# Performance work log

Hardware: AMD Instinct MI355X
Metric: run time of the kernel (lower is better)

Reference implementation:

```python
import jax, jax.numpy as jnp
import numpy as np

B, T, D, H = 1, 4096, 1024, 16
HD = D // H          # head_dim = 64
W_LOCAL = 256        # sliding-window half-width (hardcoded in module)
N_GLOBAL = 64        # number of global tokens (hardcoded in module)


def setup_inputs() -> dict:
    key = jax.random.key(0)
    ks = jax.random.split(key, 7)
    s = 0.02
    return {
        "hidden_states": jax.random.normal(ks[0], (B, T, D), dtype=jnp.float32),
        "Wqkv": jax.random.normal(ks[1], (D, 3 * D), dtype=jnp.float32) * s,
        "bqkv": jnp.zeros((3 * D,), dtype=jnp.float32),
        "Wout": jax.random.normal(ks[2], (D, D), dtype=jnp.float32) * s,
        "bout": jnp.zeros((D,), dtype=jnp.float32),
        "Wg": jax.random.normal(ks[3], (D, 1), dtype=jnp.float32) * s,
        "bg": jnp.zeros((1,), dtype=jnp.float32),
    }


def reference(hidden_states, Wqkv, bqkv, Wout, bout, Wg, bg):
    b, t, d = hidden_states.shape
    scale = 1.0 / jnp.sqrt(jnp.asarray(HD, hidden_states.dtype))

    qkv = hidden_states @ Wqkv + bqkv                     # [B,T,3D]
    q, k, v = jnp.split(qkv, 3, axis=-1)
    # [B,T,D] -> [B,H,T,HD]
    q, k, v = (x.reshape(b, t, H, HD).transpose(0, 2, 1, 3) for x in (q, k, v))

    # local sliding-window attention (dense scores masked to |i-j| <= w, as in source)
    idx = jnp.arange(t)
    local_mask = jnp.abs(idx[None, :] - idx[:, None]) <= W_LOCAL   # [T,T]
    scores = jnp.einsum('bhqd,bhkd->bhqk', q, k) * scale           # [B,H,T,T]
    scores = jnp.where(local_mask[None, None], scores, -jnp.inf)
    attn_local = jnp.einsum('bhqk,bhkd->bhqd', jax.nn.softmax(scores, axis=-1), v)

    # global-token attention: every query attends to the first N_GLOBAL tokens
    ng = min(N_GLOBAL, t)
    k_g = k[:, :, :ng, :]                                          # [B,H,G,HD]
    v_g = v[:, :, :ng, :]
    scores_g = jnp.einsum('bhqd,bhgd->bhqg', q, k_g) * scale       # [B,H,T,G]
    attn_global = jnp.einsum('bhqg,bhgd->bhqd', jax.nn.softmax(scores_g, axis=-1), v_g)

    # sigmoid gate combine, broadcast over heads and head_dim
    gate = jax.nn.sigmoid(hidden_states @ Wg + bg).reshape(b, 1, t, 1)
    out = (1.0 - gate) * attn_local + gate * attn_global           # [B,H,T,HD]
    out = out.transpose(0, 2, 1, 3).reshape(b, t, d)
    return out @ Wout + bout
```

## Files before the change

### kernel.cpp

```cpp
#include <hip/hip_runtime.h>

typedef _Float16 half8 __attribute__((ext_vector_type(8)));
typedef _Float16 half4_t __attribute__((ext_vector_type(4)));
typedef float f32x4 __attribute__((ext_vector_type(4)));

#define MFMA(a, b, c) __builtin_amdgcn_mfma_f32_16x16x32_f16(a, b, c, 0, 0, 0)

constexpr int T_TOK = 4096;
constexpr int DMODEL = 1024;
constexpr int WLOC = 256;

typedef const __attribute__((address_space(1))) uint32_t* gptr_t;
typedef __attribute__((address_space(3))) uint32_t* lptr_t;
static __device__ __forceinline__ void gl16(const void* g, void* l) {
  __builtin_amdgcn_global_load_lds((gptr_t)g, (lptr_t)l, 16, 0, 0);
}

__global__ __launch_bounds__(256) void k_cast(const float* __restrict__ in,
                                              _Float16* __restrict__ out) {
  int i = (blockIdx.x * 256 + threadIdx.x) * 8;
  f32x4 a = *(const f32x4*)(in + i);
  f32x4 b = *(const f32x4*)(in + i + 4);
  half8 h;
  h[0] = (_Float16)a[0]; h[1] = (_Float16)a[1]; h[2] = (_Float16)a[2]; h[3] = (_Float16)a[3];
  h[4] = (_Float16)b[0]; h[5] = (_Float16)b[1]; h[6] = (_Float16)b[2]; h[7] = (_Float16)b[3];
  *(half8*)(out + i) = h;
}

__global__ __launch_bounds__(256) void k_transpose_cast(const float* __restrict__ in,
                                                        _Float16* __restrict__ out,
                                                        int R, int C) {
  __shared__ float tile[64][65];
  int r0 = blockIdx.y * 64, c0 = blockIdx.x * 64;
  int tr = threadIdx.x >> 4;
  int tc = (threadIdx.x & 15) * 4;
#pragma unroll
  for (int p = 0; p < 4; ++p) {
    int r = p * 16 + tr;
    f32x4 v = *(const f32x4*)&in[(size_t)(r0 + r) * C + c0 + tc];
    tile[r][tc + 0] = v[0]; tile[r][tc + 1] = v[1];
    tile[r][tc + 2] = v[2]; tile[r][tc + 3] = v[3];
  }
  __syncthreads();
#pragma unroll
  for (int p = 0; p < 4; ++p) {
    int c = p * 16 + tr;
    half4_t h;
    h[0] = (_Float16)tile[tc + 0][c];
    h[1] = (_Float16)tile[tc + 1][c];
    h[2] = (_Float16)tile[tc + 2][c];
    h[3] = (_Float16)tile[tc + 3][c];
    *(half4_t*)&out[(size_t)(c0 + c) * R + r0 + tc] = h;
  }
}

__global__ __launch_bounds__(256) void k_gate(const float* __restrict__ hs,
                                              const float* __restrict__ Wg,
                                              const float* __restrict__ bg,
                                              float* __restrict__ gate) {
  int t = blockIdx.x * 4 + (threadIdx.x >> 6);
  int lane = threadIdx.x & 63;
  float s = 0.f;
#pragma unroll
  for (int i = 0; i < 16; ++i)
    s += hs[(size_t)t * DMODEL + lane + i * 64] * Wg[lane + i * 64];
#pragma unroll
  for (int off = 32; off; off >>= 1) s += __shfl_xor(s, off);
  if (lane == 0) gate[t] = 1.f / (1.f + __expf(-(s + bg[0])));
}

template <int MODE>
__global__ __launch_bounds__(256) void k_gemm(const _Float16* __restrict__ A,
                                              const _Float16* __restrict__ Bt,
                                              const float* __restrict__ bias,
                                              float* __restrict__ Cout,
                                              _Float16* __restrict__ qh,
                                              _Float16* __restrict__ kh,
                                              _Float16* __restrict__ vt,
                                              int M, int N, int K) {
  __shared__ __align__(16) _Float16 As[128][32];
  __shared__ __align__(16) _Float16 Bs[128][32];
  int tid = threadIdx.x;
  int lane = tid & 63, wave = tid >> 6;
  int wm = wave >> 1, wn = wave & 1;
  int m0 = blockIdx.y * 128, n0 = blockIdx.x * 128;
  int lr = lane & 15, lk = (lane >> 4) * 8;
  int sr = tid >> 2, sc = (tid & 3) * 8;
  f32x4 acc[4][4] = {};

  for (int kt = 0; kt < K; kt += 32) {
    __syncthreads();
    gl16(&A[(size_t)(m0 + sr) * K + kt + sc],       &As[sr][sc]);
    gl16(&A[(size_t)(m0 + sr + 64) * K + kt + sc],  &As[sr + 64][sc]);
    gl16(&Bt[(size_t)(n0 + sr) * K + kt + sc],      &Bs[sr][sc]);
    gl16(&Bt[(size_t)(n0 + sr + 64) * K + kt + sc], &Bs[sr + 64][sc]);
    __syncthreads();
    half8 af[4], bf[4];
#pragma unroll
    for (int i = 0; i < 4; ++i) af[i] = *(half8*)&As[wm * 64 + i * 16 + lr][lk];
#pragma unroll
    for (int i = 0; i < 4; ++i) bf[i] = *(half8*)&Bs[wn * 64 + i * 16 + lr][lk];
#pragma unroll
    for (int i = 0; i < 4; ++i)
#pragma unroll
      for (int j = 0; j < 4; ++j)
        acc[i][j] = MFMA(af[i], bf[j], acc[i][j]);
  }

  int lg2 = lane >> 4;
#pragma unroll
  for (int j = 0; j < 4; ++j) {
    int n = n0 + wn * 64 + j * 16 + lr;
    float b = bias[n];
#pragma unroll
    for (int i = 0; i < 4; ++i) {
#pragma unroll
      for (int r = 0; r < 4; ++r) {
        int m = m0 + wm * 64 + i * 16 + lg2 * 4 + r;
        float v = acc[i][j][r] + b;
        if (MODE == 1) {
          Cout[(size_t)m * N + n] = v;
        } else {
          int hh = (n >> 6) & 15, d = n & 63;
          if (n < 1024)      qh[((size_t)hh * T_TOK + m) * 64 + d] = (_Float16)v;
          else if (n < 2048) kh[((size_t)hh * T_TOK + m) * 64 + d] = (_Float16)v;
          else               vt[((size_t)hh * 64 + d) * T_TOK + m] = (_Float16)v;
        }
      }
    }
  }
}

__global__ __launch_bounds__(256) void k_attn(const _Float16* __restrict__ q_all,
                                              const _Float16* __restrict__ k_all,
                                              const _Float16* __restrict__ vT_all,
                                              const float* __restrict__ gate,
                                              _Float16* __restrict__ attn_h) {
  __shared__ __align__(16) _Float16 Ks[64][72];
  __shared__ __align__(16) _Float16 Vs[64][72];
  __shared__ __align__(16) _Float16 P[4][16][80];

  int n = blockIdx.x;
  int o = (n & 7) * 128 + (n >> 3);
  int h = o >> 6, qb = o & 63;
  int q0 = qb * 64;
  int tid = threadIdx.x;
  int lane = tid & 63, w = tid >> 6;
  int lr = lane & 15, lgp = lane >> 4;

  const _Float16* qh = q_all + (size_t)h * T_TOK * 64;
  const _Float16* kh = k_all + (size_t)h * T_TOK * 64;
  const _Float16* vt = vT_all + (size_t)h * 64 * T_TOK;

  int qrow = q0 + w * 16 + lr;
  half8 aq0 = *(const half8*)&qh[(size_t)qrow * 64 + lgp * 8];
  half8 aq1 = *(const half8*)&qh[(size_t)qrow * 64 + 32 + lgp * 8];

  int r8 = tid >> 3, c8 = (tid & 7) * 8;

  f32x4 acc_g[4] = {}, acc_l[4] = {};
  float m_g[4], l_g[4], m_l[4], l_l[4];
#pragma unroll
  for (int r = 0; r < 4; ++r) { m_g[r] = m_l[r] = -1e30f; l_g[r] = l_l[r] = 0.f; }

  auto stage = [&](int key0) {
    half8 k0 = *(const half8*)&kh[(size_t)(key0 + r8) * 64 + c8];
    half8 k1 = *(const half8*)&kh[(size_t)(key0 + r8 + 32) * 64 + c8];
    half8 v0 = *(const half8*)&vt[(size_t)r8 * T_TOK + key0 + c8];
    half8 v1 = *(const half8*)&vt[(size_t)(r8 + 32) * T_TOK + key0 + c8];
    *(half8*)&Ks[r8][c8] = k0;
    *(half8*)&Ks[r8 + 32][c8] = k1;
    *(half8*)&Vs[r8][c8] = v0;
    *(half8*)&Vs[r8 + 32][c8] = v1;
  };

  auto compute = [&](int key0, bool use_mask, f32x4 (&acc)[4], float (&ms)[4], float (&ls)[4]) {
    f32x4 s[4] = {};
#pragma unroll
    for (int g = 0; g < 4; ++g) {
      half8 b0 = *(half8*)&Ks[g * 16 + lr][lgp * 8];
      half8 b1 = *(half8*)&Ks[g * 16 + lr][32 + lgp * 8];
      s[g] = MFMA(aq0, b0, s[g]);
      s[g] = MFMA(aq1, b1, s[g]);
    }
    float sc[4][4];
#pragma unroll
    for (int g = 0; g < 4; ++g)
#pragma unroll
      for (int r = 0; r < 4; ++r) sc[g][r] = s[g][r] * 0.125f;
    if (use_mask) {
#pragma unroll
      for (int g = 0; g < 4; ++g)
#pragma unroll
        for (int r = 0; r < 4; ++r) {
          int key = key0 + g * 16 + lr, q = q0 + w * 16 + lgp * 4 + r;
          if (key < q - WLOC || key > q + WLOC) sc[g][r] = -1e30f;
        }
    }
    float mx[4];
#pragma unroll
    for (int r = 0; r < 4; ++r)
      mx[r] = fmaxf(fmaxf(sc[0][r], sc[1][r]), fmaxf(sc[2][r], sc[3][r]));
#pragma unroll
    for (int off = 1; off < 16; off <<= 1)
#pragma unroll
      for (int r = 0; r < 4; ++r) mx[r] = fmaxf(mx[r], __shfl_xor(mx[r], off));
    float al[4];
#pragma unroll
    for (int r = 0; r < 4; ++r) {
      float mn = fmaxf(ms[r], mx[r]);
      al[r] = __expf(ms[r] - mn);
      ms[r] = mn;
    }
    float pv[4][4], rs[4] = {0.f, 0.f, 0.f, 0.f};
#pragma unroll
    for (int g = 0; g < 4; ++g)
#pragma unroll
      for (int r = 0; r < 4; ++r) {
        float x = sc[g][r];
        float p = (x > -9e29f) ? __expf(x - ms[r]) : 0.f;
        pv[g][r] = p;
        rs[r] += p;
      }
#pragma unroll
    for (int off = 1; off < 16; off <<= 1)
#pragma unroll
      for (int r = 0; r < 4; ++r) rs[r] += __shfl_xor(rs[r], off);
#pragma unroll
    for (int r = 0; r < 4; ++r) ls[r] = ls[r] * al[r] + rs[r];
#pragma unroll
    for (int dt = 0; dt < 4; ++dt)
#pragma unroll
      for (int r = 0; r < 4; ++r) acc[dt][r] *= al[r];
#pragma unroll
    for (int g = 0; g < 4; ++g)
#pragma unroll
      for (int r = 0; r < 4; ++r) P[w][lgp * 4 + r][g * 16 + lr] = (_Float16)pv[g][r];
    half8 pa0 = *(half8*)&P[w][lr][lgp * 8];
    half8 pa1 = *(half8*)&P[w][lr][32 + lgp * 8];
#pragma unroll
    for (int dt = 0; dt < 4; ++dt) {
      half8 bv0 = *(half8*)&Vs[dt * 16 + lr][lgp * 8];
      half8 bv1 = *(half8*)&Vs[dt * 16 + lr][32 + lgp * 8];
      acc[dt] = MFMA(pa0, bv0, acc[dt]);
      acc[dt] = MFMA(pa1, bv1, acc[dt]);
    }
  };

  stage(0);
  __syncthreads();
  compute(0, false, acc_g, m_g, l_g);

  int lo = q0 - WLOC; if (lo < 0) lo = 0;
  int hi = q0 + 63 + WLOC + 1; if (hi > T_TOK) hi = T_TOK;
  for (int key0 = lo; key0 < hi; key0 += 64) {
    __syncthreads();
    stage(key0);
    __syncthreads();
    compute(key0, true, acc_l, m_l, l_l);
  }

#pragma unroll
  for (int r = 0; r < 4; ++r) {
    int q = q0 + w * 16 + lgp * 4 + r;
    float g = gate[q];
#pragma unroll
    for (int dt = 0; dt < 4; ++dt) {
      float o2 = (1.f - g) * (acc_l[dt][r] / l_l[r]) + g * (acc_g[dt][r] / l_g[r]);
      attn_h[(size_t)q * DMODEL + h * 64 + dt * 16 + lr] = (_Float16)o2;
    }
  }
}

extern "C" void kernel_launch(void* const* d_in, const int* in_sizes, int n_in,
                              void* d_out, int out_size, void* d_ws, size_t ws_size,
                              hipStream_t stream) {
  const float* hs   = (const float*)d_in[0];
  const float* Wqkv = (const float*)d_in[1];
  const float* bqkv = (const float*)d_in[2];
  const float* Wout = (const float*)d_in[3];
  const float* bout = (const float*)d_in[4];
  const float* Wg   = (const float*)d_in[5];
  const float* bg   = (const float*)d_in[6];
  float* out = (float*)d_out;

  char* ws = (char*)d_ws;
  _Float16* hidden_h = (_Float16*)(ws);
  _Float16* Wqkv_t   = (_Float16*)(ws + 8388608);
  _Float16* Wout_t   = (_Float16*)(ws + 14680064);
  _Float16* q_h      = (_Float16*)(ws + 16777216);
  _Float16* k_h      = (_Float16*)(ws + 25165824);
  _Float16* vT_h     = (_Float16*)(ws + 33554432);
  float*    gate     = (float*)(ws + 41943040);
  _Float16* attn_h   = hidden_h;

  k_cast<<<2048, 256, 0, stream>>>(hs, hidden_h);
  k_gate<<<1024, 256, 0, stream>>>(hs, Wg, bg, gate);
  k_transpose_cast<<<dim3(48, 16), 256, 0, stream>>>(Wqkv, Wqkv_t, 1024, 3072);
  k_transpose_cast<<<dim3(16, 16), 256, 0, stream>>>(Wout, Wout_t, 1024, 1024);
  k_gemm<0><<<dim3(24, 32), 256, 0, stream>>>(hidden_h, Wqkv_t, bqkv, nullptr,
                                              q_h, k_h, vT_h, 4096, 3072, 1024);
  k_attn<<<1024, 256, 0, stream>>>(q_h, k_h, vT_h, gate, attn_h);
  k_gemm<1><<<dim3(8, 32), 256, 0, stream>>>(attn_h, Wout_t, bout, out,
                                             nullptr, nullptr, nullptr, 4096, 1024, 1024);
}
```

Measured before the change: 215.1 us.

## Prefetch K/V into registers and restructure attention softmax per lane

The attention kernel now loads the next K/V tile into registers while computing the current one, then writes it to LDS, replacing the serial load-sync-compute loop. It swaps the MFMA operand order so each lane owns a single query row, which cuts the row max/sum reductions to two cross-lane shuffles. It also rescales only when the max grows, skips masking for interior tiles, and pre-scales Q in fp16 so the per-score multiply disappears. The risks are higher register pressure, a slightly different rounding from the fp16 Q scaling, and some extra shuffles in the epilogue.

```diff
diff --git a/kernel.cpp b/kernel.cpp
--- a/kernel.cpp
+++ b/kernel.cpp
@@ -138,7 +138,7 @@
                                               _Float16* __restrict__ attn_h) {
   __shared__ __align__(16) _Float16 Ks[64][72];
   __shared__ __align__(16) _Float16 Vs[64][72];
-  __shared__ __align__(16) _Float16 P[4][16][80];
+  __shared__ __align__(16) _Float16 P[4][16][72];
 
   int n = blockIdx.x;
   int o = (n & 7) * 128 + (n >> 3);
@@ -152,90 +152,88 @@
   const _Float16* kh = k_all + (size_t)h * T_TOK * 64;
   const _Float16* vt = vT_all + (size_t)h * 64 * T_TOK;
 
-  int qrow = q0 + w * 16 + lr;
-  half8 aq0 = *(const half8*)&qh[(size_t)qrow * 64 + lgp * 8];
-  half8 aq1 = *(const half8*)&qh[(size_t)qrow * 64 + 32 + lgp * 8];
+  half8 aq0 = *(const half8*)&qh[(size_t)(q0 + w * 16 + lr) * 64 + lgp * 8];
+  half8 aq1 = *(const half8*)&qh[(size_t)(q0 + w * 16 + lr) * 64 + 32 + lgp * 8];
+#pragma unroll
+  for (int j = 0; j < 8; ++j) { aq0[j] = aq0[j] * (_Float16)0.125f; aq1[j] = aq1[j] * (_Float16)0.125f; }
 
   int r8 = tid >> 3, c8 = (tid & 7) * 8;
+  half8 kr0, kr1, vr0, vr1;
+
+  auto ldregs = [&](int key0) {
+    kr0 = *(const half8*)&kh[(size_t)(key0 + r8) * 64 + c8];
+    kr1 = *(const half8*)&kh[(size_t)(key0 + r8 + 32) * 64 + c8];
+    vr0 = *(const half8*)&vt[(size_t)r8 * T_TOK + key0 + c8];
+    vr1 = *(const half8*)&vt[(size_t)(r8 + 32) * T_TOK + key0 + c8];
+  };
+  auto dswrite = [&]() {
+    *(half8*)&Ks[r8][c8]      = kr0;
+    *(half8*)&Ks[r8 + 32][c8] = kr1;
+    *(half8*)&Vs[r8][c8]      = vr0;
+    *(half8*)&Vs[r8 + 32][c8] = vr1;
+  };
 
   f32x4 acc_g[4] = {}, acc_l[4] = {};
-  float m_g[4], l_g[4], m_l[4], l_l[4];
-#pragma unroll
-  for (int r = 0; r < 4; ++r) { m_g[r] = m_l[r] = -1e30f; l_g[r] = l_l[r] = 0.f; }
-
-  auto stage = [&](int key0) {
-    half8 k0 = *(const half8*)&kh[(size_t)(key0 + r8) * 64 + c8];
-    half8 k1 = *(const half8*)&kh[(size_t)(key0 + r8 + 32) * 64 + c8];
-    half8 v0 = *(const half8*)&vt[(size_t)r8 * T_TOK + key0 + c8];
-    half8 v1 = *(const half8*)&vt[(size_t)(r8 + 32) * T_TOK + key0 + c8];
-    *(half8*)&Ks[r8][c8] = k0;
-    *(half8*)&Ks[r8 + 32][c8] = k1;
-    *(half8*)&Vs[r8][c8] = v0;
-    *(half8*)&Vs[r8 + 32][c8] = v1;
-  };
-
-  auto compute = [&](int key0, bool use_mask, f32x4 (&acc)[4], float (&ms)[4], float (&ls)[4]) {
+  float m_g = -1e30f, l_g = 0.f, m_l = -1e30f, l_l = 0.f;
+
+  auto compute = [&](int key0, bool use_mask, f32x4 (&acc)[4], float& ms, float& ls) {
     f32x4 s[4] = {};
 #pragma unroll
     for (int g = 0; g < 4; ++g) {
       half8 b0 = *(half8*)&Ks[g * 16 + lr][lgp * 8];
       half8 b1 = *(half8*)&Ks[g * 16 + lr][32 + lgp * 8];
-      s[g] = MFMA(aq0, b0, s[g]);
-      s[g] = MFMA(aq1, b1, s[g]);
-    }
-    float sc[4][4];
+      s[g] = MFMA(b0, aq0, s[g]);
+      s[g] = MFMA(b1, aq1, s[g]);
+    }
+    if (use_mask) {
+      int moff = key0 + lgp * 4 - (q0 + w * 16 + lr) + WLOC;
+#pragma unroll
+      for (int g = 0; g < 4; ++g)
+#pragma unroll
+        for (int r = 0; r < 4; ++r) {
+          unsigned u = (unsigned)(moff + g * 16 + r);
+          if (u > 2u * WLOC) s[g][r] = -1e30f;
+        }
+    }
+    float mloc = -1e30f;
 #pragma unroll
     for (int g = 0; g < 4; ++g)
 #pragma unroll
-      for (int r = 0; r < 4; ++r) sc[g][r] = s[g][r] * 0.125f;
-    if (use_mask) {
-#pragma unroll
-      for (int g = 0; g < 4; ++g)
-#pragma unroll
-        for (int r = 0; r < 4; ++r) {
-          int key = key0 + g * 16 + lr, q = q0 + w * 16 + lgp * 4 + r;
-          if (key < q - WLOC || key > q + WLOC) sc[g][r] = -1e30f;
-        }
-    }
-    float mx[4];
-#pragma unroll
-    for (int r = 0; r < 4; ++r)
-      mx[r] = fmaxf(fmaxf(sc[0][r], sc[1][r]), fmaxf(sc[2][r], sc[3][r]));
-#pragma unroll
-    for (int off = 1; off < 16; off <<= 1)
-#pragma unroll
-      for (int r = 0; r < 4; ++r) mx[r] = fmaxf(mx[r], __shfl_xor(mx[r], off));
-    float al[4];
-#pragma unroll
-    for (int r = 0; r < 4; ++r) {
-      float mn = fmaxf(ms[r], mx[r]);
-      al[r] = __expf(ms[r] - mn);
-      ms[r] = mn;
-    }
-    float pv[4][4], rs[4] = {0.f, 0.f, 0.f, 0.f};
+      for (int r = 0; r < 4; ++r) mloc = fmaxf(mloc, s[g][r]);
+    mloc = fmaxf(mloc, __shfl_xor(mloc, 16));
+    mloc = fmaxf(mloc, __shfl_xor(mloc, 32));
+    if (__any(mloc > ms)) {
+      float mn = fmaxf(ms, mloc);
+      float al = __expf(ms - mn);
+      ms = mn;
+      float alr[4];
+#pragma unroll
+      for (int r = 0; r < 4; ++r) alr[r] = __shfl(al, lgp * 4 + r);
+#pragma unroll
+      for (int dt = 0; dt < 4; ++dt)
+#pragma unroll
+        for (int r = 0; r < 4; ++r) acc[dt][r] *= alr[r];
+      ls *= al;
+    }
+    float rsum = 0.f;
 #pragma unroll
     for (int g = 0; g < 4; ++g)
 #pragma unroll
       for (int r = 0; r < 4; ++r) {
-        float x = sc[g][r];
-        float p = (x > -9e29f) ? __expf(x - ms[r]) : 0.f;
-        pv[g][r] = p;
-        rs[r] += p;
+        float p = __expf(s[g][r] - ms);
+        s[g][r] = p;
+        rsum += p;
       }
-#pragma unroll
-    for (int off = 1; off < 16; off <<= 1)
-#pragma unroll
-      for (int r = 0; r < 4; ++r) rs[r] += __shfl_xor(rs[r], off);
-#pragma unroll
-    for (int r = 0; r < 4; ++r) ls[r] = ls[r] * al[r] + rs[r];
-#pragma unroll
-    for (int dt = 0; dt < 4; ++dt)
-#pragma unroll
-      for (int r = 0; r < 4; ++r) acc[dt][r] *= al[r];
-#pragma unroll
-    for (int g = 0; g < 4; ++g)
-#pragma unroll
-      for (int r = 0; r < 4; ++r) P[w][lgp * 4 + r][g * 16 + lr] = (_Float16)pv[g][r];
+    rsum += __shfl_xor(rsum, 16);
+    rsum += __shfl_xor(rsum, 32);
+    ls += rsum;
+#pragma unroll
+    for (int g = 0; g < 4; ++g) {
+      half4_t q4;
+      q4[0] = (_Float16)s[g][0]; q4[1] = (_Float16)s[g][1];
+      q4[2] = (_Float16)s[g][2]; q4[3] = (_Float16)s[g][3];
+      *(half4_t*)&P[w][lr][g * 16 + lgp * 4] = q4;
+    }
     half8 pa0 = *(half8*)&P[w][lr][lgp * 8];
     half8 pa1 = *(half8*)&P[w][lr][32 + lgp * 8];
 #pragma unroll
@@ -247,26 +245,40 @@
     }
   };
 
-  stage(0);
+  ldregs(0);
+  dswrite();
   __syncthreads();
-  compute(0, false, acc_g, m_g, l_g);
-
   int lo = q0 - WLOC; if (lo < 0) lo = 0;
   int hi = q0 + 63 + WLOC + 1; if (hi > T_TOK) hi = T_TOK;
+  ldregs(lo);
+  compute(0, false, acc_g, m_g, l_g);
+  __syncthreads();
+  dswrite();
+  __syncthreads();
+
   for (int key0 = lo; key0 < hi; key0 += 64) {
+    int nxt = key0 + 64;
+    bool have_nxt = nxt < hi;
+    if (have_nxt) ldregs(nxt);
+    bool use_mask = (key0 < q0 - 192) || (key0 > q0 + 192);
+    compute(key0, use_mask, acc_l, m_l, l_l);
     __syncthreads();
-    stage(key0);
-    __syncthreads();
-    compute(key0, true, acc_l, m_l, l_l);
-  }
-
+    if (have_nxt) { dswrite(); __syncthreads(); }
+  }
+
+  float llr[4], lgr[4];
+#pragma unroll
+  for (int r = 0; r < 4; ++r) {
+    llr[r] = __shfl(l_l, lgp * 4 + r);
+    lgr[r] = __shfl(l_g, lgp * 4 + r);
+  }
 #pragma unroll
   for (int r = 0; r < 4; ++r) {
     int q = q0 + w * 16 + lgp * 4 + r;
     float g = gate[q];
 #pragma unroll
     for (int dt = 0; dt < 4; ++dt) {
-      float o2 = (1.f - g) * (acc_l[dt][r] / l_l[r]) + g * (acc_g[dt][r] / l_g[r]);
+      float o2 = (1.f - g) * (acc_l[dt][r] / llr[r]) + g * (acc_g[dt][r] / lgr[r]);
       attn_h[(size_t)q * DMODEL + h * 64 + dt * 16 + lr] = (_Float16)o2;
     }
   }
```

Result: faster. 200.1 us (-7.0%).
